# Kernel tuning notes

Hardware: AMD Instinct MI355X
Metric: run time of the kernel (lower is better)

Reference implementation:

```python
import jax, jax.numpy as jnp
import numpy as np

B, T, V, C, NB = 8, 2048, 1024, 128, 32


def setup_inputs() -> dict:
    key = jax.random.key(0)
    ks = jax.random.split(key, 6)
    x = jax.random.normal(ks[0], (B, T, V), jnp.float32)
    basis = jax.random.normal(ks[1], (V, 2 * NB), jnp.float32)
    q_coeffs = jax.random.normal(ks[2], (C, 2 * NB), jnp.float32) * 0.02
    k_coeffs = jax.random.normal(ks[3], (C, 2 * NB), jnp.float32) * 0.02
    v_coeffs = jax.random.normal(ks[4], (C, 2 * NB), jnp.float32) * 0.02
    o_coeffs = jax.random.normal(ks[5], (C, 2 * NB), jnp.float32) * 0.02
    decay = jnp.float32(0.95)
    out_scale = jnp.float32(0.1)
    return {"x": x, "basis": basis, "q_coeffs": q_coeffs, "k_coeffs": k_coeffs,
            "v_coeffs": v_coeffs, "o_coeffs": o_coeffs, "decay": decay, "out_scale": out_scale}


def reference(x, basis, q_coeffs, k_coeffs, v_coeffs, o_coeffs, decay, out_scale):
    # Fourier-parameterized projections: (V, C); softmax over vocab dim for q/k/v
    q_w = jax.nn.softmax(basis @ q_coeffs.T, axis=0)
    k_w = jax.nn.softmax(basis @ k_coeffs.T, axis=0)
    v_w = jax.nn.softmax(basis @ v_coeffs.T, axis=0)
    o_w = basis @ o_coeffs.T  # (V, C), no softmax

    q = x @ q_w  # (B, T, C)
    k = x @ k_w
    v = x @ v_w
    d = jax.nn.sigmoid(decay)

    M0 = jnp.zeros((x.shape[0], q_w.shape[1], q_w.shape[1]), x.dtype)  # (B, C, C)

    def step(M, qkv_t):
        q_t, k_t, v_t = qkv_t  # each (B, C)
        retrieved = jnp.einsum('bc,bcd->bd', q_t, M)  # read BEFORE write (as in torch loop)
        M_new = d * M + jnp.einsum('bc,bd->bcd', k_t, v_t)
        return M_new, retrieved

    qT = jnp.swapaxes(q, 0, 1)  # (T, B, C)
    kT = jnp.swapaxes(k, 0, 1)
    vT = jnp.swapaxes(v, 0, 1)
    _, rs = jax.lax.scan(step, M0, (qT, kT, vT))  # rs: (T, B, C)
    retrieved = jnp.swapaxes(rs, 0, 1)  # (B, T, C)
    return (retrieved @ o_w.T) * out_scale  # (B, T, V)
```

## Files before the change

### kernel.cpp

```cpp
#include <hip/hip_runtime.h>
#include <math.h>

#define B_   8
#define T_   2048
#define V_   1024
#define C_   128
#define NB2  64
#define L_   32
#define NC_  64

typedef _Float16 f16_t;
typedef f16_t f16x8 __attribute__((ext_vector_type(8)));
typedef float f32x4 __attribute__((ext_vector_type(4)));

__device__ __forceinline__ float sigmoidf_(float x){ return 1.0f/(1.0f+expf(-x)); }

__device__ __forceinline__ void gload_lds16(const void* g, void* l){
  __builtin_amdgcn_global_load_lds(
      (const __attribute__((address_space(1))) uint32_t*)g,
      (__attribute__((address_space(3))) uint32_t*)l, 16, 0, 0);
}

__global__ __launch_bounds__(256) void weights_kernel(
    const float* __restrict__ basis,
    const float* __restrict__ qc, const float* __restrict__ kc,
    const float* __restrict__ vc, const float* __restrict__ oc,
    f16_t* __restrict__ Wo, f16_t* __restrict__ Wt)
{
  int blk  = blockIdx.x;
  int proj = blk >> 7;
  int c    = blk & 127;
  const float* coeffs = (proj==0)?qc : (proj==1)?kc : (proj==2)?vc : oc;

  __shared__ float coef[NB2];
  __shared__ float red[256];
  int tid = threadIdx.x;
  if (tid < NB2) coef[tid] = coeffs[c*NB2 + tid];
  __syncthreads();

  float l[4];
  for (int i=0;i<4;i++){
    int v = tid + i*256;
    const float4* bp = (const float4*)(basis + (size_t)v*NB2);
    float s = 0.f;
    #pragma unroll
    for (int f=0; f<NB2/4; f++){
      float4 b4 = bp[f];
      s += b4.x*coef[f*4+0] + b4.y*coef[f*4+1] + b4.z*coef[f*4+2] + b4.w*coef[f*4+3];
    }
    l[i] = s;
  }
  if (proj == 3){
    for (int i=0;i<4;i++){ int v = tid+i*256; Wo[(size_t)v*C_ + c] = (f16_t)l[i]; }
    return;
  }
  float mx = fmaxf(fmaxf(l[0],l[1]), fmaxf(l[2],l[3]));
  red[tid] = mx; __syncthreads();
  for (int s=128; s>0; s>>=1){ if (tid<s) red[tid] = fmaxf(red[tid], red[tid+s]); __syncthreads(); }
  mx = red[0]; __syncthreads();
  float sum = 0.f;
  for (int i=0;i<4;i++) sum += expf(l[i]-mx);
  red[tid] = sum; __syncthreads();
  for (int s=128; s>0; s>>=1){ if (tid<s) red[tid] += red[tid+s]; __syncthreads(); }
  float inv = 1.0f/red[0];
  f16_t* tp = Wt + ((size_t)proj*C_ + c)*V_;
  for (int i=0;i<4;i++){
    int v = tid+i*256;
    tp[v] = (f16_t)(expf(l[i]-mx)*inv);
  }
}

#define BM 64
#define BMP 32
#define BN 128
#define BK 64
#define PADK 72
#define NF_  384
#define NT_PROJ (V_/BK)

__global__ __launch_bounds__(512, 1) void proj_fused_kernel(
    const float* __restrict__ x,
    const f16_t* __restrict__ Wt,
    float* __restrict__ out)
{
  const int M = B_*T_;
  int m0 = blockIdx.x * BMP;

  __shared__ __align__(16) f16_t As[BMP][PADK];
  __shared__ __align__(16) f16_t Bsh[NF_*BK];

  int tid  = threadIdx.x;
  int lane = tid & 63;
  int w    = tid >> 6;
  int wm   = (w >> 2) * 16;
  int wn   = (w & 3) * 96;
  int lr   = lane & 15;
  int lg   = lane >> 4;

  const float* xbase = x + (size_t)m0*V_;

  f32x4 acc[6] = {};

  for (int kt = 0; kt < NT_PROJ; kt++){
    #pragma unroll
    for (int i=0;i<6;i++){
      int ci = i*512 + tid;
      int r  = ci >> 3, ch = ci & 7;
      const f16_t* src = Wt + (size_t)r*V_ + kt*BK + ((ch ^ (r&7))<<3);
      gload_lds16(src, &Bsh[ci*8]);
    }
    {
      int row = tid >> 4, qq = tid & 15;
      float4 xv = *(const float4*)(xbase + (size_t)row*V_ + kt*BK + qq*4);
      union { f16_t h[4]; ushort4 u; } hh;
      hh.h[0]=(f16_t)xv.x; hh.h[1]=(f16_t)xv.y; hh.h[2]=(f16_t)xv.z; hh.h[3]=(f16_t)xv.w;
      *(ushort4*)&As[row][qq*4] = hh.u;
    }
    __syncthreads();

    #pragma unroll
    for (int kh=0; kh<2; kh++){
      f16x8 a = *(f16x8*)&As[wm + lr][kh*32 + lg*8];
      #pragma unroll
      for (int nt=0; nt<6; nt++){
        int n  = wn + nt*16 + lr;
        int c0 = kh*4 + lg;
        f16x8 b = *(f16x8*)&Bsh[n*BK + ((c0 ^ (n&7))<<3)];
        acc[nt] = __builtin_amdgcn_mfma_f32_16x16x32_f16(a, b, acc[nt], 0,0,0);
      }
    }
    __syncthreads();
  }

  #pragma unroll
  for (int nt=0; nt<6; nt++){
    int n   = wn + nt*16 + lr;
    int p   = n >> 7;
    int col = n & 127;
    float* op = out + (size_t)p*M*C_;
    #pragma unroll
    for (int r=0; r<4; r++){
      int row = m0 + wm + lg*4 + r;
      op[(size_t)row*C_ + col] = acc[nt][r];
    }
  }
}

__global__ __launch_bounds__(256) void kvsum_kernel(
    const float* __restrict__ k, const float* __restrict__ v,
    const float* __restrict__ dptr, float* __restrict__ kv)
{
  int ci = blockIdx.x, b = blockIdx.y;
  float d = sigmoidf_(dptr[0]);
  __shared__ float ks[L_][132];
  __shared__ float vs[L_][132];
  int tid = threadIdx.x;
  const float* kp = k + ((size_t)b*T_ + ci*L_)*C_;
  const float* vp = v + ((size_t)b*T_ + ci*L_)*C_;
  #pragma unroll
  for (int i=0;i<4;i++){
    int idx = tid + i*256;
    int j = idx >> 5, c4 = idx & 31;
    float w = powf(d, (float)(L_-1-j));
    float4 k4 = *(const float4*)(kp + (size_t)j*C_ + c4*4);
    k4.x*=w; k4.y*=w; k4.z*=w; k4.w*=w;
    *(float4*)&ks[j][c4*4] = k4;
    *(float4*)&vs[j][c4*4] = *(const float4*)(vp + (size_t)j*C_ + c4*4);
  }
  __syncthreads();
  int tc = tid >> 4, td = tid & 15;
  float acc[8][8] = {};
  for (int j=0;j<L_;j++){
    float kr[8], vr[8];
    *(float4*)&kr[0] = *(float4*)&ks[j][tc*8];
    *(float4*)&kr[4] = *(float4*)&ks[j][tc*8+4];
    *(float4*)&vr[0] = *(float4*)&vs[j][td*8];
    *(float4*)&vr[4] = *(float4*)&vs[j][td*8+4];
    #pragma unroll
    for (int a=0;a<8;a++)
      #pragma unroll
      for (int bb=0;bb<8;bb++) acc[a][bb] += kr[a]*vr[bb];
  }
  float* op = kv + ((size_t)b*NC_ + ci)*C_*C_;
  for (int a=0;a<8;a++)
    for (int b4=0;b4<2;b4++)
      *(float4*)(op + (size_t)(tc*8+a)*C_ + td*8 + b4*4) =
        make_float4(acc[a][b4*4],acc[a][b4*4+1],acc[a][b4*4+2],acc[a][b4*4+3]);
}

__global__ __launch_bounds__(256) void scan_kernel(
    float* __restrict__ kv, const float* __restrict__ dptr)
{
  int idx = blockIdx.x*256 + threadIdx.x;
  int b = idx >> 14, e = idx & 16383;
  float d  = sigmoidf_(dptr[0]);
  float dL = powf(d, (float)L_);
  float* p = kv + (size_t)b*NC_*C_*C_ + e;
  const size_t S = (size_t)C_*C_;
  float m = 0.f;
  #pragma unroll 4
  for (int g=0; g<NC_/4; g++){
    float s0 = p[(size_t)(4*g+0)*S];
    float s1 = p[(size_t)(4*g+1)*S];
    float s2 = p[(size_t)(4*g+2)*S];
    float s3 = p[(size_t)(4*g+3)*S];
    p[(size_t)(4*g+0)*S] = m;  m = dL*m + s0;
    p[(size_t)(4*g+1)*S] = m;  m = dL*m + s1;
    p[(size_t)(4*g+2)*S] = m;  m = dL*m + s2;
    p[(size_t)(4*g+3)*S] = m;  m = dL*m + s3;
  }
}

__global__ __launch_bounds__(256) void intra_kernel(
    const float* __restrict__ q, const float* __restrict__ k,
    const float* __restrict__ v, const float* __restrict__ Minit,
    const float* __restrict__ dptr,
    f16_t* __restrict__ ret)
{
  int ci = blockIdx.x, b = blockIdx.y;
  int tid = threadIdx.x;
  float d = sigmoidf_(dptr[0]);
  __shared__ float qs[L_][132];
  __shared__ float kvs[L_][132];
  __shared__ __align__(16) float Ms[C_][C_];
  __shared__ float ps[L_][33];
  __shared__ float dpow[L_+1];
  if (tid <= L_) dpow[tid] = powf(d, (float)tid);

  const float* qp = q + ((size_t)b*T_ + ci*L_)*C_;
  const float* kp = k + ((size_t)b*T_ + ci*L_)*C_;
  const float* vp = v + ((size_t)b*T_ + ci*L_)*C_;
  const float* Mp = Minit + ((size_t)b*NC_ + ci)*C_*C_;

  #pragma unroll
  for (int i=0;i<16;i++){
    int cidx = i*256 + tid;
    gload_lds16(Mp + (size_t)cidx*4, &Ms[0][0] + cidx*4);
  }
  #pragma unroll
  for (int i=0;i<4;i++){
    int idx = tid + i*256;
    int j = idx >> 5, c4 = idx & 31;
    *(float4*)&qs[j][c4*4]  = *(const float4*)(qp + (size_t)j*C_ + c4*4);
    *(float4*)&kvs[j][c4*4] = *(const float4*)(kp + (size_t)j*C_ + c4*4);
  }
  __syncthreads();

  {
    int tr = tid >> 4, tj = tid & 15;
    float s[2][2] = {};
    for (int c4=0;c4<32;c4++){
      float4 q4[2], k4[2];
      #pragma unroll
      for (int i=0;i<2;i++) q4[i] = *(float4*)&qs[tr*2+i][c4*4];
      #pragma unroll
      for (int i=0;i<2;i++) k4[i] = *(float4*)&kvs[tj*2+i][c4*4];
      #pragma unroll
      for (int a=0;a<2;a++)
        #pragma unroll
        for (int bb=0;bb<2;bb++)
          s[a][bb] += q4[a].x*k4[bb].x + q4[a].y*k4[bb].y + q4[a].z*k4[bb].z + q4[a].w*k4[bb].w;
    }
    #pragma unroll
    for (int a=0;a<2;a++)
      #pragma unroll
      for (int bb=0;bb<2;bb++){
        int r = tr*2+a, j = tj*2+bb;
        ps[r][j] = (j < r) ? s[a][bb]*dpow[r-1-j] : 0.f;
      }
  }
  __syncthreads();

  #pragma unroll
  for (int i=0;i<4;i++){
    int idx = tid + i*256;
    int j = idx >> 5, c4 = idx & 31;
    *(float4*)&kvs[j][c4*4] = *(const float4*)(vp + (size_t)j*C_ + c4*4);
  }

  int tx = tid & 31, ty = tid >> 5;
  float acc[4][4] = {};
  for (int c=0;c<C_;c++){
    float4 m4 = *(const float4*)&Ms[c][tx*4];
    #pragma unroll
    for (int r=0;r<4;r++){
      float qv = qs[ty*4+r][c];
      acc[r][0] += qv*m4.x; acc[r][1] += qv*m4.y; acc[r][2] += qv*m4.z; acc[r][3] += qv*m4.w;
    }
  }
  #pragma unroll
  for (int r=0;r<4;r++){
    float sc = dpow[ty*4+r];
    #pragma unroll
    for (int j=0;j<4;j++) acc[r][j] *= sc;
  }
  __syncthreads();

  for (int j=0;j<L_;j++){
    float4 v4 = *(float4*)&kvs[j][tx*4];
    #pragma unroll
    for (int r=0;r<4;r++){
      float p = ps[ty*4+r][j];
      acc[r][0] += p*v4.x; acc[r][1] += p*v4.y; acc[r][2] += p*v4.z; acc[r][3] += p*v4.w;
    }
  }
  size_t rbase = ((size_t)b*T_ + ci*L_)*C_;
  for (int r=0;r<4;r++){
    union { f16_t h[4]; ushort4 u; } hh;
    #pragma unroll
    for (int j=0;j<4;j++) hh.h[j] = (f16_t)acc[r][j];
    *(ushort4*)(ret + rbase + (size_t)(ty*4+r)*C_ + tx*4) = hh.u;
  }
}

__global__ __launch_bounds__(256) void out_mfma_kernel(
    const f16_t* __restrict__ A, const f16_t* __restrict__ Bw,
    const float* __restrict__ scl, float* __restrict__ out)
{
  int m0 = blockIdx.x * BM;
  int n0 = blockIdx.y * BN;
  float osc = scl[0];

  int tid  = threadIdx.x;
  int lane = tid & 63;
  int w    = tid >> 6;
  int wm   = (w >> 1) * 32;
  int wn   = (w & 1) * 64;
  int lr   = lane & 15;
  int lg   = lane >> 4;

  f32x4 acc[2][4] = {};

  #pragma unroll
  for (int kh=0; kh<4; kh++){
    f16x8 a[2];
    #pragma unroll
    for (int mt=0; mt<2; mt++)
      a[mt] = *(const f16x8*)(A + (size_t)(m0 + wm + mt*16 + lr)*C_ + kh*32 + lg*8);
    #pragma unroll
    for (int nt=0; nt<4; nt++){
      f16x8 bfr = *(const f16x8*)(Bw + (size_t)(n0 + wn + nt*16 + lr)*C_ + kh*32 + lg*8);
      #pragma unroll
      for (int mt=0; mt<2; mt++)
        acc[mt][nt] = __builtin_amdgcn_mfma_f32_16x16x32_f16(a[mt], bfr, acc[mt][nt], 0,0,0);
    }
  }

  #pragma unroll
  for (int mt=0; mt<2; mt++)
    #pragma unroll
    for (int nt=0; nt<4; nt++)
      #pragma unroll
      for (int r=0; r<4; r++){
        int row = m0 + wm + mt*16 + lg*4 + r;
        int col = n0 + wn + nt*16 + lr;
        out[(size_t)row*V_ + col] = acc[mt][nt][r] * osc;
      }
}

extern "C" void kernel_launch(void* const* d_in, const int* in_sizes, int n_in,
                              void* d_out, int out_size, void* d_ws, size_t ws_size,
                              hipStream_t stream)
{
  const float* x     = (const float*)d_in[0];
  const float* basis = (const float*)d_in[1];
  const float* qc    = (const float*)d_in[2];
  const float* kc    = (const float*)d_in[3];
  const float* vc    = (const float*)d_in[4];
  const float* oc    = (const float*)d_in[5];
  const float* dptr  = (const float*)d_in[6];
  const float* sptr  = (const float*)d_in[7];
  float* out = (float*)d_out;
  float* ws  = (float*)d_ws;

  const size_t M = (size_t)B_*T_;
  f16_t* Wo  = (f16_t*)ws;
  f16_t* Wt  = (f16_t*)(ws + 65536);
  float* qkv = ws + 262144;
  f16_t* ret = (f16_t*)(ws + 6553600);
  float* kv  = ws + 7602176;

  float* q = qkv;
  float* k = qkv + M*C_;
  float* v = qkv + 2*M*C_;

  hipLaunchKernelGGL(weights_kernel, dim3(512), dim3(256), 0, stream,
                     basis, qc, kc, vc, oc, Wo, Wt);
  hipLaunchKernelGGL(proj_fused_kernel, dim3(512), dim3(512), 0, stream,
                     x, Wt, qkv);
  hipLaunchKernelGGL(kvsum_kernel, dim3(NC_, B_), dim3(256), 0, stream, k, v, dptr, kv);
  hipLaunchKernelGGL(scan_kernel, dim3(512), dim3(256), 0, stream, kv, dptr);
  hipLaunchKernelGGL(intra_kernel, dim3(NC_, B_), dim3(256), 0, stream,
                     q, k, v, kv, dptr, ret);
  hipLaunchKernelGGL(out_mfma_kernel, dim3(256, 8), dim3(256), 0, stream,
                     ret, Wo, sptr, out);
}
```

Measured before the change: 271.0 us.

## Double-buffer LDS and enlarge row tile in fused QKV projection kernel

```diff
diff --git a/kernel.cpp b/kernel.cpp
--- a/kernel.cpp
+++ b/kernel.cpp
@@ -71,7 +71,6 @@
 }
 
 #define BM 64
-#define BMP 32
 #define BN 128
 #define BK 64
 #define PADK 72
@@ -84,66 +83,88 @@
     float* __restrict__ out)
 {
   const int M = B_*T_;
-  int m0 = blockIdx.x * BMP;
-
-  __shared__ __align__(16) f16_t As[BMP][PADK];
-  __shared__ __align__(16) f16_t Bsh[NF_*BK];
+  int m0 = blockIdx.x * BM;
+
+  __shared__ __align__(16) f16_t As[2][BM][PADK];
+  __shared__ __align__(16) f16_t Bsh[2][NF_*BK];
 
   int tid  = threadIdx.x;
   int lane = tid & 63;
   int w    = tid >> 6;
-  int wm   = (w >> 2) * 16;
+  int wm   = (w >> 2) * 32;
   int wn   = (w & 3) * 96;
   int lr   = lane & 15;
   int lg   = lane >> 4;
 
   const float* xbase = x + (size_t)m0*V_;
 
-  f32x4 acc[6] = {};
-
-  for (int kt = 0; kt < NT_PROJ; kt++){
-    #pragma unroll
-    for (int i=0;i<6;i++){
-      int ci = i*512 + tid;
-      int r  = ci >> 3, ch = ci & 7;
-      const f16_t* src = Wt + (size_t)r*V_ + kt*BK + ((ch ^ (r&7))<<3);
-      gload_lds16(src, &Bsh[ci*8]);
-    }
-    {
-      int row = tid >> 4, qq = tid & 15;
-      float4 xv = *(const float4*)(xbase + (size_t)row*V_ + kt*BK + qq*4);
-      union { f16_t h[4]; ushort4 u; } hh;
-      hh.h[0]=(f16_t)xv.x; hh.h[1]=(f16_t)xv.y; hh.h[2]=(f16_t)xv.z; hh.h[3]=(f16_t)xv.w;
-      *(ushort4*)&As[row][qq*4] = hh.u;
-    }
+  f32x4 acc[2][6] = {};
+
+#define PROJ_STAGE(buf, kt) do { \
+    _Pragma("unroll") \
+    for (int i=0;i<6;i++){ \
+      int ci = i*512 + tid; \
+      int r  = ci >> 3, ch = ci & 7; \
+      const f16_t* src = Wt + (size_t)r*V_ + (kt)*BK + ((ch ^ (r&7))<<3); \
+      gload_lds16(src, &Bsh[buf][ci*8]); \
+    } \
+    _Pragma("unroll") \
+    for (int i=0;i<2;i++){ \
+      int ci = i*512 + tid; \
+      int row = ci >> 4, qq = ci & 15; \
+      float4 xv = *(const float4*)(xbase + (size_t)row*V_ + (kt)*BK + qq*4); \
+      union { f16_t h[4]; ushort4 u; } hh; \
+      hh.h[0]=(f16_t)xv.x; hh.h[1]=(f16_t)xv.y; \
+      hh.h[2]=(f16_t)xv.z; hh.h[3]=(f16_t)xv.w; \
+      *(ushort4*)&As[buf][row][qq*4] = hh.u; \
+    } \
+  } while(0)
+
+#define PROJ_COMPUTE(buf) do { \
+    _Pragma("unroll") \
+    for (int kh=0; kh<2; kh++){ \
+      f16x8 a[2]; \
+      _Pragma("unroll") \
+      for (int mt=0; mt<2; mt++) \
+        a[mt] = *(f16x8*)&As[buf][wm + mt*16 + lr][kh*32 + lg*8]; \
+      _Pragma("unroll") \
+      for (int nt=0; nt<6; nt++){ \
+        int n  = wn + nt*16 + lr; \
+        int c0 = kh*4 + lg; \
+        f16x8 b = *(f16x8*)&Bsh[buf][n*BK + ((c0 ^ (n&7))<<3)]; \
+        _Pragma("unroll") \
+        for (int mt=0; mt<2; mt++) \
+          acc[mt][nt] = __builtin_amdgcn_mfma_f32_16x16x32_f16(a[mt], b, acc[mt][nt], 0,0,0); \
+      } \
+    } \
+  } while(0)
+
+  PROJ_STAGE(0, 0);
+  __syncthreads();
+  for (int kt=1; kt<NT_PROJ; kt++){
+    PROJ_STAGE(kt&1, kt);
+    PROJ_COMPUTE((kt-1)&1);
     __syncthreads();
-
-    #pragma unroll
-    for (int kh=0; kh<2; kh++){
-      f16x8 a = *(f16x8*)&As[wm + lr][kh*32 + lg*8];
-      #pragma unroll
-      for (int nt=0; nt<6; nt++){
-        int n  = wn + nt*16 + lr;
-        int c0 = kh*4 + lg;
-        f16x8 b = *(f16x8*)&Bsh[n*BK + ((c0 ^ (n&7))<<3)];
-        acc[nt] = __builtin_amdgcn_mfma_f32_16x16x32_f16(a, b, acc[nt], 0,0,0);
+  }
+  PROJ_COMPUTE(1);
+
+#undef PROJ_STAGE
+#undef PROJ_COMPUTE
+
+  #pragma unroll
+  for (int mt=0; mt<2; mt++)
+    #pragma unroll
+    for (int nt=0; nt<6; nt++){
+      int n   = wn + nt*16 + lr;
+      int p   = n >> 7;
+      int col = n & 127;
+      float* op = out + (size_t)p*M*C_;
+      #pragma unroll
+      for (int r=0; r<4; r++){
+        int row = m0 + wm + mt*16 + lg*4 + r;
+        op[(size_t)row*C_ + col] = acc[mt][nt][r];
       }
     }
-    __syncthreads();
-  }
-
-  #pragma unroll
-  for (int nt=0; nt<6; nt++){
-    int n   = wn + nt*16 + lr;
-    int p   = n >> 7;
-    int col = n & 127;
-    float* op = out + (size_t)p*M*C_;
-    #pragma unroll
-    for (int r=0; r<4; r++){
-      int row = m0 + wm + lg*4 + r;
-      op[(size_t)row*C_ + col] = acc[nt][r];
-    }
-  }
 }
 
 __global__ __launch_bounds__(256) void kvsum_kernel(
@@ -386,7 +407,7 @@
 
   hipLaunchKernelGGL(weights_kernel, dim3(512), dim3(256), 0, stream,
                      basis, qc, kc, vc, oc, Wo, Wt);
-  hipLaunchKernelGGL(proj_fused_kernel, dim3(512), dim3(512), 0, stream,
+  hipLaunchKernelGGL(proj_fused_kernel, dim3(256), dim3(512), 0, stream,
                      x, Wt, qkv);
   hipLaunchKernelGGL(kvsum_kernel, dim3(NC_, B_), dim3(256), 0, stream, k, v, dptr, kv);
   hipLaunchKernelGGL(scan_kernel, dim3(512), dim3(256), 0, stream, kv, dptr);
```

Measured after the change: 257.1 us. 5.1% less time.
